# Optimization experiments

Hardware: AMD Instinct MI355X
Metric: run time of the kernel (lower is better)

## Reference

```python
import jax, jax.numpy as jnp
import numpy as np

N, E = 50000, 800000
DIN, DH, DOUT = 128, 128, 64


def setup_inputs() -> dict:
    key = jax.random.key(0)
    ks = jax.random.split(key, 18)
    s = 0.05
    inp = {
        "x": jax.random.normal(ks[0], (N, DIN), dtype=jnp.float32),
        "edge_index": jax.random.randint(ks[1], (2, E), 0, N, dtype=jnp.int64),
        # conv1 MLP: Linear(DIN,DH), Linear(DH,DH)
        "c1_w1": jax.random.normal(ks[2], (DIN, DH), dtype=jnp.float32) * s,
        "c1_b1": jax.random.normal(ks[3], (DH,), dtype=jnp.float32) * s,
        "c1_w2": jax.random.normal(ks[4], (DH, DH), dtype=jnp.float32) * s,
        "c1_b2": jax.random.normal(ks[5], (DH,), dtype=jnp.float32) * s,
        # conv2 MLP
        "c2_w1": jax.random.normal(ks[6], (DH, DH), dtype=jnp.float32) * s,
        "c2_b1": jax.random.normal(ks[7], (DH,), dtype=jnp.float32) * s,
        "c2_w2": jax.random.normal(ks[8], (DH, DH), dtype=jnp.float32) * s,
        "c2_b2": jax.random.normal(ks[9], (DH,), dtype=jnp.float32) * s,
        # conv3 MLP
        "c3_w1": jax.random.normal(ks[10], (DH, DH), dtype=jnp.float32) * s,
        "c3_b1": jax.random.normal(ks[11], (DH,), dtype=jnp.float32) * s,
        "c3_w2": jax.random.normal(ks[12], (DH, DH), dtype=jnp.float32) * s,
        "c3_b2": jax.random.normal(ks[13], (DH,), dtype=jnp.float32) * s,
        # output head
        "lin1_w": jax.random.normal(ks[14], (DH, DH), dtype=jnp.float32) * s,
        "lin1_b": jax.random.normal(ks[15], (DH,), dtype=jnp.float32) * s,
        "lin2_w": jax.random.normal(ks[16], (DH, DOUT), dtype=jnp.float32) * s,
        "lin2_b": jax.random.normal(ks[17], (DOUT,), dtype=jnp.float32) * s,
    }
    return inp


def _gin_conv(h, src, dst, w1, b1, w2, b2):
    # PyG GINConv, eps=0: MLP((1+eps)*x + sum_{j->i} x_j)
    agg = jax.ops.segment_sum(h[src], dst, num_segments=h.shape[0])  # [N, D]
    z = h + agg
    z = jax.nn.relu(z @ w1 + b1)
    return jax.nn.relu(z @ w2 + b2)


def reference(x, edge_index, c1_w1, c1_b1, c1_w2, c1_b2,
              c2_w1, c2_b1, c2_w2, c2_b2,
              c3_w1, c3_b1, c3_w2, c3_b2,
              lin1_w, lin1_b, lin2_w, lin2_b):
    src, dst = edge_index[0], edge_index[1]
    h = _gin_conv(x, src, dst, c1_w1, c1_b1, c1_w2, c1_b2)
    h = jax.nn.relu(h)  # redundant after MLP ReLU, but faithful to source
    h = _gin_conv(h, src, dst, c2_w1, c2_b1, c2_w2, c2_b2)
    h = jax.nn.relu(h)
    h = _gin_conv(h, src, dst, c3_w1, c3_b1, c3_w2, c3_b2)
    h = jax.nn.relu(h @ lin1_w + lin1_b)
    return h @ lin2_w + lin2_b  # [N, DOUT]
```

## Files before the change

kernel.cpp:

```cpp
#include <hip/hip_runtime.h>
#include <hip/hip_bf16.h>

typedef __attribute__((ext_vector_type(8))) short bf16x8;
typedef __attribute__((ext_vector_type(4))) float f32x4;

#define DH 128
#define DOUT 64

static __device__ __forceinline__ unsigned short f2bf(float f) {
    __hip_bfloat16 h = __float2bfloat16(f);
    return *(unsigned short*)&h;
}
static __device__ __forceinline__ void acc2(float& a0, float& a1, unsigned int u) {
    a0 += __uint_as_float(u << 16);
    a1 += __uint_as_float(u & 0xffff0000u);
}
static __device__ __forceinline__ void accq(float* a, const uint4& u) {
    acc2(a[0], a[1], u.x);
    acc2(a[2], a[3], u.y);
    acc2(a[4], a[5], u.z);
    acc2(a[6], a[7], u.w);
}


struct WPrep {
    const float* src[8];
    unsigned short* dst[8];
};

__global__ void prep_kernel(const float* __restrict__ x, unsigned short* __restrict__ xb,
                            unsigned short* __restrict__ hA, unsigned short* __restrict__ hB,
                            int n4, WPrep p, int* __restrict__ cnt,
                            int* __restrict__ esrc, int Epad, int N_) {
    int id = blockIdx.x * blockDim.x + threadIdx.x;
    if (id < n4) {
        float4 v = ((const float4*)x)[id];
        ushort4 b;
        b.x = f2bf(v.x); b.y = f2bf(v.y); b.z = f2bf(v.z); b.w = f2bf(v.w);
        ((ushort4*)xb)[id] = b;
        return;
    }
    id -= n4;
    if (id < N_) { cnt[id] = 0; return; }
    id -= N_;
    if (id < 7 * 16384 + 8192) {
        int m, off;
        if (id < 7 * 16384) { m = id >> 14; off = id & 16383; }
        else { m = 7; off = id - 7 * 16384; }
        int shift = (m == 7) ? 6 : 7;
        int nc = 1 << shift;
        int k = off >> shift;
        int n = off & (nc - 1);
        p.dst[m][n * 128 + k] = f2bf(p.src[m][off]);
        return;
    }
    id -= 7 * 16384 + 8192;
    if (id < 3 * 128) {
        int j = id & 127, w = id >> 7;
        if (w == 0) xb[(size_t)N_ * 128 + j] = 0;
        else if (w == 1) hA[(size_t)N_ * 128 + j] = 0;
        else hB[(size_t)N_ * 128 + j] = 0;
        return;
    }
    id -= 384;
    if (id < Epad) esrc[id] = N_;
}


__global__ void hist_kernel(const int* __restrict__ dst, int* __restrict__ cnt,
                            int* __restrict__ rank, int E, int n) {
    int e = blockIdx.x * blockDim.x + threadIdx.x;
    if (e < E) {
        int d = dst[e];
        if ((unsigned)d < (unsigned)n) rank[e] = atomicAdd(&cnt[d], 1);
    }
}

__global__ void scan1_kernel(const int* __restrict__ cnt, int* __restrict__ rp_part,
                             int* __restrict__ bsum, int n) {
    __shared__ int s[256];
    int tid = threadIdx.x;
    int i = blockIdx.x * 256 + tid;
    int v = (i < n) ? ((cnt[i] + 15) & ~15) : 0;
    s[tid] = v;
    __syncthreads();
    for (int off = 1; off < 256; off <<= 1) {
        int t = (tid >= off) ? s[tid - off] : 0;
        __syncthreads();
        s[tid] += t;
        __syncthreads();
    }
    if (i <= n) rp_part[i] = s[tid] - v;
    if (tid == 255) bsum[blockIdx.x] = s[255];
}

__global__ void scan2_kernel(int* __restrict__ bsum, int nb) {
    __shared__ int s[256];
    int tid = threadIdx.x;
    int v = (tid < nb) ? bsum[tid] : 0;
    s[tid] = v;
    __syncthreads();
    for (int off = 1; off < 256; off <<= 1) {
        int t = (tid >= off) ? s[tid - off] : 0;
        __syncthreads();
        s[tid] += t;
        __syncthreads();
    }
    if (tid < nb) bsum[tid] = s[tid] - v;
}

__global__ void scan3_fill_kernel(const int* __restrict__ rp_part, const int* __restrict__ bsum,
                                  int* __restrict__ row_ptr,
                                  const int* __restrict__ src, const int* __restrict__ dst,
                                  const int* __restrict__ rank, int* __restrict__ esrc,
                                  int n, int E) {
    int gid = blockIdx.x * blockDim.x + threadIdx.x;
    if (gid <= n) row_ptr[gid] = rp_part[gid] + bsum[gid >> 8];
    if (gid < E) {
        int d = dst[gid];
        if ((unsigned)d < (unsigned)n)
            esrc[rp_part[d] + bsum[d >> 8] + rank[gid]] = src[gid];
    }
}


template <bool HEAD>
__launch_bounds__(256, 4)
__global__ void layer_kernel(const unsigned short* __restrict__ h,
                             const int* __restrict__ rp,
                             const int* __restrict__ esrc,
                             const unsigned short* __restrict__ W1t,
                             const float* __restrict__ b1,
                             const unsigned short* __restrict__ W2t,
                             const float* __restrict__ b2,
                             const unsigned short* __restrict__ W3t,
                             const float* __restrict__ b3,
                             const unsigned short* __restrict__ W4t,
                             const float* __restrict__ b4,
                             void* __restrict__ outp, int M) {
    constexpr int LDA = 128 + 8;
    __shared__ __align__(16) unsigned short As[16][LDA];
    __shared__ __align__(16) unsigned short Zs[16][LDA];

    int tid = threadIdx.x;
    int wave = __builtin_amdgcn_readfirstlane(tid >> 6);
    int lane = tid & 63;
    int grp = lane >> 4;
    int c = lane & 15;
    int row0 = blockIdx.x * 16;
    int nd0 = row0 + wave * 4;

    const uint4* hq = (const uint4*)h;

    uint4 s[4];
#pragma unroll
    for (int i = 0; i < 4; ++i) s[i] = hq[(nd0 + i) * 16 + c];

    int b[4], rn[4];
#pragma unroll
    for (int i = 0; i < 4; ++i) {
        int rb = rp[nd0 + i], re = rp[nd0 + i + 1];
        b[i] = rb;
        rn[i] = (re - rb) >> 4;
    }

    float acc[4][8];
#pragma unroll
    for (int i = 0; i < 4; ++i)
#pragma unroll
        for (int j = 0; j < 8; ++j) acc[i][j] = 0.f;

    if (grp == 0) {
#pragma unroll
        for (int i = 0; i < 4; ++i) accq(acc[i], s[i]);
    }

    int maxr = max(max(rn[0], rn[1]), max(rn[2], rn[3]));
    for (int r = 0; r < maxr; ++r) {
#pragma unroll
        for (int half = 0; half < 2; ++half) {
            int idx[8];
#pragma unroll
            for (int t = 0; t < 8; ++t) {
                int i = half * 2 + (t >> 2);
                idx[t] = esrc[b[i] + (r << 4) + ((t & 3) << 2) + grp];
            }
#pragma unroll
            for (int t = 0; t < 8; ++t) {
                int i = half * 2 + (t >> 2);
                idx[t] = (r < rn[i]) ? idx[t] : M;
            }
            uint4 u[8];
#pragma unroll
            for (int t = 0; t < 8; ++t) u[t] = hq[idx[t] * 16 + c];
#pragma unroll
            for (int t = 0; t < 8; ++t) accq(acc[half * 2 + (t >> 2)], u[t]);
        }
    }

#pragma unroll
    for (int i = 0; i < 4; ++i) {
#pragma unroll
        for (int j = 0; j < 8; ++j) {
            float v = acc[i][j];
            v += __shfl_xor(v, 16, 64);
            v += __shfl_xor(v, 32, 64);
            acc[i][j] = v;
        }
        if (grp == 0) {
            uint4 ov;
            ov.x = (unsigned)f2bf(acc[i][0]) | ((unsigned)f2bf(acc[i][1]) << 16);
            ov.y = (unsigned)f2bf(acc[i][2]) | ((unsigned)f2bf(acc[i][3]) << 16);
            ov.z = (unsigned)f2bf(acc[i][4]) | ((unsigned)f2bf(acc[i][5]) << 16);
            ov.w = (unsigned)f2bf(acc[i][6]) | ((unsigned)f2bf(acc[i][7]) << 16);
            *(uint4*)(&As[wave * 4 + i][c * 8]) = ov;
        }
    }
    __syncthreads();

    int quad = lane >> 4;
    int l16 = lane & 15;

    bf16x8 af[4];
#pragma unroll
    for (int kt = 0; kt < 4; ++kt)
        af[kt] = *(const bf16x8*)(&As[l16][kt * 32 + quad * 8]);
#pragma unroll
    for (int p = 0; p < 2; ++p) {
        int ncol = (wave * 2 + p) * 16 + l16;
        const unsigned short* wp = W1t + ncol * 128 + quad * 8;
        f32x4 a = {0.f, 0.f, 0.f, 0.f};
#pragma unroll
        for (int kt = 0; kt < 4; ++kt)
            a = __builtin_amdgcn_mfma_f32_16x16x32_bf16(
                af[kt], *(const bf16x8*)(wp + kt * 32), a, 0, 0, 0);
        float bs = b1[ncol];
#pragma unroll
        for (int r = 0; r < 4; ++r) {
            float v = a[r] + bs;
            if (v < 0.f) v = 0.f;
            Zs[quad * 4 + r][ncol] = f2bf(v);
        }
    }
    __syncthreads();

    bf16x8 zf[4];
#pragma unroll
    for (int kt = 0; kt < 4; ++kt)
        zf[kt] = *(const bf16x8*)(&Zs[l16][kt * 32 + quad * 8]);
#pragma unroll
    for (int p = 0; p < 2; ++p) {
        int ncol = (wave * 2 + p) * 16 + l16;
        const unsigned short* wp = W2t + ncol * 128 + quad * 8;
        f32x4 a = {0.f, 0.f, 0.f, 0.f};
#pragma unroll
        for (int kt = 0; kt < 4; ++kt)
            a = __builtin_amdgcn_mfma_f32_16x16x32_bf16(
                zf[kt], *(const bf16x8*)(wp + kt * 32), a, 0, 0, 0);
        float bs = b2[ncol];
#pragma unroll
        for (int r = 0; r < 4; ++r) {
            float v = a[r] + bs;
            if (v < 0.f) v = 0.f;
            if (HEAD) {
                As[quad * 4 + r][ncol] = f2bf(v);
            } else {
                int grow = row0 + quad * 4 + r;
                if (grow < M)
                    ((unsigned short*)outp)[(size_t)grow * 128 + ncol] = f2bf(v);
            }
        }
    }

    if (HEAD) {
        __syncthreads();
        bf16x8 hf[4];
#pragma unroll
        for (int kt = 0; kt < 4; ++kt)
            hf[kt] = *(const bf16x8*)(&As[l16][kt * 32 + quad * 8]);
#pragma unroll
        for (int p = 0; p < 2; ++p) {
            int ncol = (wave * 2 + p) * 16 + l16;
            const unsigned short* wp = W3t + ncol * 128 + quad * 8;
            f32x4 a = {0.f, 0.f, 0.f, 0.f};
#pragma unroll
            for (int kt = 0; kt < 4; ++kt)
                a = __builtin_amdgcn_mfma_f32_16x16x32_bf16(
                    hf[kt], *(const bf16x8*)(wp + kt * 32), a, 0, 0, 0);
            float bs = b3[ncol];
#pragma unroll
            for (int r = 0; r < 4; ++r) {
                float v = a[r] + bs;
                if (v < 0.f) v = 0.f;
                Zs[quad * 4 + r][ncol] = f2bf(v);
            }
        }
        __syncthreads();
        bf16x8 gf[4];
#pragma unroll
        for (int kt = 0; kt < 4; ++kt)
            gf[kt] = *(const bf16x8*)(&Zs[l16][kt * 32 + quad * 8]);
        {
            int ncol = wave * 16 + l16;
            const unsigned short* wp = W4t + ncol * 128 + quad * 8;
            f32x4 a = {0.f, 0.f, 0.f, 0.f};
#pragma unroll
            for (int kt = 0; kt < 4; ++kt)
                a = __builtin_amdgcn_mfma_f32_16x16x32_bf16(
                    gf[kt], *(const bf16x8*)(wp + kt * 32), a, 0, 0, 0);
            float bs = b4[ncol];
#pragma unroll
            for (int r = 0; r < 4; ++r) {
                int grow = row0 + quad * 4 + r;
                if (grow < M)
                    ((float*)outp)[(size_t)grow * 64 + ncol] = a[r] + bs;
            }
        }
    }
}


extern "C" void kernel_launch(void* const* d_in, const int* in_sizes, int n_in,
                              void* d_out, int out_size, void* d_ws, size_t ws_size,
                              hipStream_t stream) {
    const float* x = (const float*)d_in[0];
    const int* ei = (const int*)d_in[1];
    int N = in_sizes[0] / DH;
    int E = in_sizes[1] / 2;
    const int* src = ei;
    const int* dstv = ei + E;
    int Epad = E + 15 * N + 1024;

    char* ws = (char*)d_ws;
    size_t off = 0;
    auto alloc = [&](size_t bytes) -> void* {
        void* p = ws + off;
        off += (bytes + 255) & ~(size_t)255;
        return p;
    };
    unsigned short* xb = (unsigned short*)alloc((size_t)(N + 1) * DH * 2);
    unsigned short* hA = (unsigned short*)alloc((size_t)(N + 1) * DH * 2);
    unsigned short* hB = (unsigned short*)alloc((size_t)(N + 1) * DH * 2);
    unsigned short* wt[8];
    for (int m = 0; m < 8; ++m) wt[m] = (unsigned short*)alloc(16384 * 2);
    int* cnt     = (int*)alloc((size_t)N * 4);
    int* rp_part = (int*)alloc((size_t)(N + 1) * 4);
    int* row_ptr = (int*)alloc((size_t)(N + 1) * 4);
    int* rank    = (int*)alloc((size_t)E * 4);
    int* bsum    = (int*)alloc(256 * 4);
    int* esrc    = (int*)alloc((size_t)Epad * 4);

    WPrep wp;
    wp.src[0] = (const float*)d_in[2];
    wp.src[1] = (const float*)d_in[4];
    wp.src[2] = (const float*)d_in[6];
    wp.src[3] = (const float*)d_in[8];
    wp.src[4] = (const float*)d_in[10];
    wp.src[5] = (const float*)d_in[12];
    wp.src[6] = (const float*)d_in[14];
    wp.src[7] = (const float*)d_in[16];
    for (int m = 0; m < 8; ++m) wp.dst[m] = wt[m];
    int n4 = N * DH / 4;
    int prep_items = n4 + N + 7 * 16384 + 8192 + 384 + Epad;
    prep_kernel<<<(prep_items + 255) / 256, 256, 0, stream>>>(
        x, xb, hA, hB, n4, wp, cnt, esrc, Epad, N);

    int nb = (N + 1 + 255) / 256;
    int eb = (E + 255) / 256;
    hist_kernel<<<eb, 256, 0, stream>>>(dstv, cnt, rank, E, N);
    scan1_kernel<<<nb, 256, 0, stream>>>(cnt, rp_part, bsum, N);
    scan2_kernel<<<1, 256, 0, stream>>>(bsum, nb);
    scan3_fill_kernel<<<eb, 256, 0, stream>>>(rp_part, bsum, row_ptr,
                                              src, dstv, rank, esrc, N, E);

    int gb = (N + 15) / 16;

    const float* c1b1 = (const float*)d_in[3];
    const float* c1b2 = (const float*)d_in[5];
    const float* c2b1 = (const float*)d_in[7];
    const float* c2b2 = (const float*)d_in[9];
    const float* c3b1 = (const float*)d_in[11];
    const float* c3b2 = (const float*)d_in[13];
    const float* l1b  = (const float*)d_in[15];
    const float* l2b  = (const float*)d_in[17];

    layer_kernel<false><<<gb, 256, 0, stream>>>(
        xb, row_ptr, esrc, wt[0], c1b1, wt[1], c1b2,
        nullptr, nullptr, nullptr, nullptr, hA, N);
    layer_kernel<false><<<gb, 256, 0, stream>>>(
        hA, row_ptr, esrc, wt[2], c2b1, wt[3], c2b2,
        nullptr, nullptr, nullptr, nullptr, hB, N);
    layer_kernel<true><<<gb, 256, 0, stream>>>(
        hB, row_ptr, esrc, wt[4], c3b1, wt[5], c3b2,
        wt[6], l1b, wt[7], l2b, d_out, N);
}
```

Baseline: 350.7 us.

## Aggregate neighbors one node per wave with scalar edge offsets

Restructures the gather-sum so each wave processes one node at a time, with all 64 lanes covering the 128-dim row (2 bf16 per lane). Edge indices are made wave-uniform through readfirstlane and stored pre-multiplied by 256 as byte offsets. The cross-lane shuffle reduction is gone and CSR padding drops from 16 to 8 entries per node. Launch bounds are raised to 8 blocks per SM. The trade-off is that nodes are handled serially within a wave, and each gather is a narrow 4-byte load per lane instead of a 16-byte load.

```diff
diff --git a/kernel.cpp b/kernel.cpp
--- a/kernel.cpp
+++ b/kernel.cpp
@@ -14,12 +14,6 @@
 static __device__ __forceinline__ void acc2(float& a0, float& a1, unsigned int u) {
     a0 += __uint_as_float(u << 16);
     a1 += __uint_as_float(u & 0xffff0000u);
-}
-static __device__ __forceinline__ void accq(float* a, const uint4& u) {
-    acc2(a[0], a[1], u.x);
-    acc2(a[2], a[3], u.y);
-    acc2(a[4], a[5], u.z);
-    acc2(a[6], a[7], u.w);
 }
 
 
@@ -63,7 +57,7 @@
         return;
     }
     id -= 384;
-    if (id < Epad) esrc[id] = N_;
+    if (id < Epad) esrc[id] = N_ << 8;
 }
 
 
@@ -81,7 +75,7 @@
     __shared__ int s[256];
     int tid = threadIdx.x;
     int i = blockIdx.x * 256 + tid;
-    int v = (i < n) ? ((cnt[i] + 15) & ~15) : 0;
+    int v = (i < n) ? ((cnt[i] + 7) & ~7) : 0;
     s[tid] = v;
     __syncthreads();
     for (int off = 1; off < 256; off <<= 1) {
@@ -119,13 +113,13 @@
     if (gid < E) {
         int d = dst[gid];
         if ((unsigned)d < (unsigned)n)
-            esrc[rp_part[d] + bsum[d >> 8] + rank[gid]] = src[gid];
+            esrc[rp_part[d] + bsum[d >> 8] + rank[gid]] = src[gid] << 8;
     }
 }
 
 
 template <bool HEAD>
-__launch_bounds__(256, 4)
+__launch_bounds__(256, 8)
 __global__ void layer_kernel(const unsigned short* __restrict__ h,
                              const int* __restrict__ rp,
                              const int* __restrict__ esrc,
@@ -145,76 +139,48 @@
     int tid = threadIdx.x;
     int wave = __builtin_amdgcn_readfirstlane(tid >> 6);
     int lane = tid & 63;
-    int grp = lane >> 4;
-    int c = lane & 15;
     int row0 = blockIdx.x * 16;
     int nd0 = row0 + wave * 4;
 
-    const uint4* hq = (const uint4*)h;
-
-    uint4 s[4];
-#pragma unroll
-    for (int i = 0; i < 4; ++i) s[i] = hq[(nd0 + i) * 16 + c];
-
-    int b[4], rn[4];
+    const char* hc = (const char*)h;
+    unsigned voff = (unsigned)lane << 2;
+
 #pragma unroll
     for (int i = 0; i < 4; ++i) {
-        int rb = rp[nd0 + i], re = rp[nd0 + i + 1];
-        b[i] = rb;
-        rn[i] = (re - rb) >> 4;
-    }
-
-    float acc[4][8];
-#pragma unroll
-    for (int i = 0; i < 4; ++i)
-#pragma unroll
-        for (int j = 0; j < 8; ++j) acc[i][j] = 0.f;
-
-    if (grp == 0) {
-#pragma unroll
-        for (int i = 0; i < 4; ++i) accq(acc[i], s[i]);
-    }
-
-    int maxr = max(max(rn[0], rn[1]), max(rn[2], rn[3]));
-    for (int r = 0; r < maxr; ++r) {
-#pragma unroll
-        for (int half = 0; half < 2; ++half) {
-            int idx[8];
-#pragma unroll
-            for (int t = 0; t < 8; ++t) {
-                int i = half * 2 + (t >> 2);
-                idx[t] = esrc[b[i] + (r << 4) + ((t & 3) << 2) + grp];
-            }
-#pragma unroll
-            for (int t = 0; t < 8; ++t) {
-                int i = half * 2 + (t >> 2);
-                idx[t] = (r < rn[i]) ? idx[t] : M;
-            }
-            uint4 u[8];
-#pragma unroll
-            for (int t = 0; t < 8; ++t) u[t] = hq[idx[t] * 16 + c];
-#pragma unroll
-            for (int t = 0; t < 8; ++t) accq(acc[half * 2 + (t >> 2)], u[t]);
-        }
-    }
-
-#pragma unroll
-    for (int i = 0; i < 4; ++i) {
-#pragma unroll
-        for (int j = 0; j < 8; ++j) {
-            float v = acc[i][j];
-            v += __shfl_xor(v, 16, 64);
-            v += __shfl_xor(v, 32, 64);
-            acc[i][j] = v;
-        }
-        if (grp == 0) {
-            uint4 ov;
-            ov.x = (unsigned)f2bf(acc[i][0]) | ((unsigned)f2bf(acc[i][1]) << 16);
-            ov.y = (unsigned)f2bf(acc[i][2]) | ((unsigned)f2bf(acc[i][3]) << 16);
-            ov.z = (unsigned)f2bf(acc[i][4]) | ((unsigned)f2bf(acc[i][5]) << 16);
-            ov.w = (unsigned)f2bf(acc[i][6]) | ((unsigned)f2bf(acc[i][7]) << 16);
-            *(uint4*)(&As[wave * 4 + i][c * 8]) = ov;
-        }
+        int nd = nd0 + i;
+        int rb = __builtin_amdgcn_readfirstlane(rp[nd]);
+        int re = __builtin_amdgcn_readfirstlane(rp[nd + 1]);
+        unsigned su = *(const unsigned*)(hc + ((size_t)(unsigned)nd << 8) + voff);
+        float a0 = 0.f, a1 = 0.f;
+        for (int r = rb; r < re; r += 8) {
+            int o0 = __builtin_amdgcn_readfirstlane(esrc[r + 0]);
+            int o1 = __builtin_amdgcn_readfirstlane(esrc[r + 1]);
+            int o2 = __builtin_amdgcn_readfirstlane(esrc[r + 2]);
+            int o3 = __builtin_amdgcn_readfirstlane(esrc[r + 3]);
+            int o4 = __builtin_amdgcn_readfirstlane(esrc[r + 4]);
+            int o5 = __builtin_amdgcn_readfirstlane(esrc[r + 5]);
+            int o6 = __builtin_amdgcn_readfirstlane(esrc[r + 6]);
+            int o7 = __builtin_amdgcn_readfirstlane(esrc[r + 7]);
+            unsigned u0 = *(const unsigned*)(hc + o0 + voff);
+            unsigned u1 = *(const unsigned*)(hc + o1 + voff);
+            unsigned u2 = *(const unsigned*)(hc + o2 + voff);
+            unsigned u3 = *(const unsigned*)(hc + o3 + voff);
+            unsigned u4 = *(const unsigned*)(hc + o4 + voff);
+            unsigned u5 = *(const unsigned*)(hc + o5 + voff);
+            unsigned u6 = *(const unsigned*)(hc + o6 + voff);
+            unsigned u7 = *(const unsigned*)(hc + o7 + voff);
+            acc2(a0, a1, u0);
+            acc2(a0, a1, u1);
+            acc2(a0, a1, u2);
+            acc2(a0, a1, u3);
+            acc2(a0, a1, u4);
+            acc2(a0, a1, u5);
+            acc2(a0, a1, u6);
+            acc2(a0, a1, u7);
+        }
+        acc2(a0, a1, su);
+        unsigned pv = (unsigned)f2bf(a0) | ((unsigned)f2bf(a1) << 16);
+        *(unsigned*)&As[wave * 4 + i][lane * 2] = pv;
     }
     __syncthreads();
 
@@ -329,7 +295,7 @@
     int E = in_sizes[1] / 2;
     const int* src = ei;
     const int* dstv = ei + E;
-    int Epad = E + 15 * N + 1024;
+    int Epad = E + 7 * N + 1024;
 
     char* ws = (char*)d_ws;
     size_t off = 0;
```

Measured after the change: 323.7 us. 1.08x faster.
